# Optimization experiments

Hardware: AMD Instinct MI355X
Metric: run time of the kernel (lower is better)

The kernel has to match this reference:

```python
import jax, jax.numpy as jnp
import numpy as np

D_MODEL = 1024
N_HEADS = 16
D_HEAD = D_MODEL // N_HEADS

def setup_inputs() -> dict:
    key = jax.random.key(0)
    k1, k2, k3 = jax.random.split(key, 3)
    x = jax.random.normal(k1, (4, 2048, D_MODEL), dtype=jnp.float32)
    # Linear weights stored as [in, out] for x @ W
    s = 1.0 / np.sqrt(D_MODEL)
    W_qkv = jax.random.uniform(k2, (D_MODEL, 3 * D_MODEL), jnp.float32, -s, s)
    W_out = jax.random.uniform(k3, (D_MODEL, D_MODEL), jnp.float32, -s, s)
    return {"x": x, "W_qkv": W_qkv, "W_out": W_out}

def reference(x, W_qkv, W_out):
    B, T, C = x.shape
    scale = D_HEAD ** -0.5
    qkv = x @ W_qkv                       # [B,T,3C]
    q, k, v = jnp.split(qkv, 3, axis=-1)
    def heads(t):
        return t.reshape(B, T, N_HEADS, D_HEAD).transpose(0, 2, 1, 3)  # [B,H,T,d]
    q, k, v = heads(q), heads(k), heads(v)
    att = jnp.einsum('bhqd,bhkd->bhqk', q, k) * scale  # [B,H,T,T]
    causal = jnp.tril(jnp.ones((T, T), dtype=bool))
    att = jnp.where(causal, att, -jnp.inf)
    att = jax.nn.softmax(att, axis=-1)
    y = jnp.einsum('bhqk,bhkd->bhqd', att, v)          # [B,H,T,d]
    y = y.transpose(0, 2, 1, 3).reshape(B, T, C)
    return y @ W_out
```

## Files before the change

### kernel.cpp

```cpp
#include <hip/hip_runtime.h>
#include <hip/hip_bf16.h>

typedef unsigned short u16;
typedef __attribute__((ext_vector_type(8))) short short8v;
typedef __attribute__((ext_vector_type(4))) float f32x4;
typedef __attribute__((ext_vector_type(16))) float f32x16;

#define Bb 4
#define Tt 2048
#define Cc 1024
#define Hh 16
#define C3 3072
#define Mm 8192

__device__ __forceinline__ u16 f2bf(float f) {
    union { __hip_bfloat16 h; u16 u; } r;
    r.h = __float2bfloat16(f);
    return r.u;
}
__device__ __forceinline__ unsigned int pk2(float a, float b) {
    union { __hip_bfloat162 h; unsigned int u; } r;
    r.h.x = __float2bfloat16(a);
    r.h.y = __float2bfloat16(b);
    return r.u;
}
__device__ __forceinline__ float exp2g(float x) {
#if __has_builtin(__builtin_amdgcn_exp2f)
    return __builtin_amdgcn_exp2f(x);
#else
    return exp2f(x);
#endif
}
__device__ __forceinline__ void plswap(unsigned int& a, unsigned int& b) {
#if __has_builtin(__builtin_amdgcn_permlane32_swap)
    typedef __attribute__((ext_vector_type(2))) unsigned int uint2v;
    uint2v r = __builtin_amdgcn_permlane32_swap(a, b, false, false);
    a = r.x; b = r.y;
#else
    asm volatile("v_permlane32_swap_b32 %0, %1" : "+v"(a), "+v"(b));
#endif
}
__device__ __forceinline__ void gload16(const void* g, void* l) {
    __builtin_amdgcn_global_load_lds(
        (const __attribute__((address_space(1))) unsigned int*)g,
        (__attribute__((address_space(3))) unsigned int*)l, 16, 0, 0);
}

__global__ __launch_bounds__(256) void cvt_x(const float* __restrict__ in,
                                             u16* __restrict__ out) {
    int i = blockIdx.x * 256 + threadIdx.x;
    float4 v = reinterpret_cast<const float4*>(in)[i];
    ushort4 o;
    o.x = f2bf(v.x); o.y = f2bf(v.y); o.z = f2bf(v.z); o.w = f2bf(v.w);
    reinterpret_cast<ushort4*>(out)[i] = o;
}

__global__ __launch_bounds__(256) void wtrans(const float* __restrict__ in,
                                              u16* __restrict__ out,
                                              int R, int Ccols) {
    __shared__ float t[32][33];
    const int tx = threadIdx.x & 31, ty = threadIdx.x >> 5;
    const int bx = blockIdx.x, by = blockIdx.y;
    const int c = bx * 32 + tx;
#pragma unroll
    for (int j = 0; j < 4; ++j) {
        int r = by * 32 + ty + j * 8;
        t[ty + j * 8][tx] = in[(size_t)r * Ccols + c];
    }
    __syncthreads();
#pragma unroll
    for (int j = 0; j < 4; ++j) {
        int orow = bx * 32 + ty + j * 8;
        int oc   = by * 32 + tx;
        out[(size_t)orow * R + oc] = f2bf(t[tx][ty + j * 8]);
    }
}

template <int MODE>
__global__ __launch_bounds__(256) void gemm_mfma(const u16* __restrict__ A,
                                                 const u16* __restrict__ BT,
                                                 void* __restrict__ C0,
                                                 u16* __restrict__ C1,
                                                 int M, int N, int K) {
    __shared__ u16 As[128 * 32];
    __shared__ u16 Bs[128 * 32];
    const int tid = threadIdx.x;
    const int w = tid >> 6, l = tid & 63;
    const int wr = w >> 1, wc = w & 1;
    const int g = l >> 4, q = l & 15;
    const int bm = blockIdx.x * 128, bn = blockIdx.y * 128;
    const int lrow = l >> 2;
    const int lcol = (l & 3) * 8;

    f32x4 acc[4][4] = {};
    const u16* Ap = A + (size_t)(bm + w * 32 + lrow) * K + lcol;
    const u16* Bp = BT + (size_t)(bn + w * 32 + lrow) * K + lcol;

    for (int k0 = 0; k0 < K; k0 += 32) {
        gload16(Ap + k0, &As[(w * 32) * 32]);
        gload16(Ap + (size_t)16 * K + k0, &As[(w * 32 + 16) * 32]);
        gload16(Bp + k0, &Bs[(w * 32) * 32]);
        gload16(Bp + (size_t)16 * K + k0, &Bs[(w * 32 + 16) * 32]);
        __syncthreads();
        short8v af[4], bf[4];
#pragma unroll
        for (int m = 0; m < 4; ++m)
            af[m] = *reinterpret_cast<const short8v*>(&As[(wr * 64 + m * 16 + q) * 32 + g * 8]);
#pragma unroll
        for (int n = 0; n < 4; ++n)
            bf[n] = *reinterpret_cast<const short8v*>(&Bs[(wc * 64 + n * 16 + q) * 32 + g * 8]);
#pragma unroll
        for (int m = 0; m < 4; ++m)
#pragma unroll
            for (int n = 0; n < 4; ++n)
                acc[m][n] = __builtin_amdgcn_mfma_f32_16x16x32_bf16(af[m], bf[n], acc[m][n], 0, 0, 0);
        __syncthreads();
    }

#pragma unroll
    for (int m = 0; m < 4; ++m)
#pragma unroll
        for (int n = 0; n < 4; ++n) {
            const int col = bn + wc * 64 + n * 16 + q;
#pragma unroll
            for (int r = 0; r < 4; ++r) {
                const int row = bm + wr * 64 + m * 16 + g * 4 + r;
                const float v = acc[m][n][r];
                if (MODE == 1) {
                    reinterpret_cast<float*>(C0)[(size_t)row * N + col] = v;
                } else if (MODE == 0) {
                    reinterpret_cast<u16*>(C0)[(size_t)row * N + col] = f2bf(v);
                } else {
                    if (col < 2048) {
                        reinterpret_cast<u16*>(C0)[(size_t)row * 2048 + col] = f2bf(v);
                    } else {
                        const int bI = row >> 11, tI = row & 2047;
                        C1[((size_t)bI * 1024 + (col - 2048)) * 2048 + tI] = f2bf(v);
                    }
                }
            }
        }
}

__global__ __launch_bounds__(256) void attn_mfma(const u16* __restrict__ qk,
                                                 const u16* __restrict__ vT,
                                                 u16* __restrict__ y) {
    __shared__ u16 SM[18432];
    const int tid = threadIdx.x;
    const int w = tid >> 6, l = tid & 63;
    const int q31 = l & 31, hi = l >> 5;
    const int bid = blockIdx.x;
    const int bh = bid & 63, c0 = bid >> 6;
    const int b = bh >> 4, h = bh & 15;
    const size_t tok0 = (size_t)b * Tt;

    const float C2 = 0.18033688011112042f;
    const float THR = 44.361419555836499f;

    const int srow = tid >> 2;
    const int sseg = (tid & 3) * 16;
    const int soff = srow * 72 + sseg;
    const u16* gK = qk + (tok0 + srow) * 2048 + 1024 + h * 64 + sseg;
    const u16* gV = vT + ((size_t)b * 1024 + h * 64 + srow) * 2048 + sseg;

    for (int phase = 0; phase < 2; ++phase) {
        const int chunk = phase ? (15 - c0) : c0;
        const int nsteps = 2 * (chunk + 1);
        const int q0w = chunk * 128 + w * 32;
        const int qlane = q0w + q31;

        short8v qf0, qf1, qf2, qf3;
        {
            const u16* qp = qk + (tok0 + qlane) * 2048 + h * 64 + hi * 8;
            qf0 = *reinterpret_cast<const short8v*>(qp);
            qf1 = *reinterpret_cast<const short8v*>(qp + 16);
            qf2 = *reinterpret_cast<const short8v*>(qp + 32);
            qf3 = *reinterpret_cast<const short8v*>(qp + 48);
        }

        f32x16 acc0 = {}, acc1 = {};
        float m_run = -1e30f, l_run = 0.f;

        {
            uint4 ka = *reinterpret_cast<const uint4*>(gK);
            uint4 kb = *reinterpret_cast<const uint4*>(gK + 8);
            uint4 va = *reinterpret_cast<const uint4*>(gV);
            uint4 vb = *reinterpret_cast<const uint4*>(gV + 8);
            *reinterpret_cast<uint4*>(&SM[soff]) = ka;
            *reinterpret_cast<uint4*>(&SM[soff + 8]) = kb;
            *reinterpret_cast<uint4*>(&SM[9216 + soff]) = va;
            *reinterpret_cast<uint4*>(&SM[9216 + soff + 8]) = vb;
        }
        __syncthreads();

        for (int t = 0; t < nsteps; ++t) {
            const int cur = t & 1;
            const int k0 = t * 64;
            const bool pre = (t + 1 < nsteps);
            uint4 ka = {}, kb = {}, va = {}, vb = {};
            if (pre) {
                const u16* gKt = gK + (size_t)(t + 1) * 64 * 2048;
                const u16* gVt = gV + (t + 1) * 64;
                ka = *reinterpret_cast<const uint4*>(gKt);
                kb = *reinterpret_cast<const uint4*>(gKt + 8);
                va = *reinterpret_cast<const uint4*>(gVt);
                vb = *reinterpret_cast<const uint4*>(gVt + 8);
            }

            if (k0 <= q0w + 31) {
                const u16* Kb = SM + cur * 4608;
                const u16* Vb = SM + 9216 + cur * 4608;
                f32x16 st0 = {}, st1 = {};
#pragma unroll
                for (int s = 0; s < 4; ++s) {
                    short8v kfa = *reinterpret_cast<const short8v*>(&Kb[q31 * 72 + s * 16 + hi * 8]);
                    short8v kfb = *reinterpret_cast<const short8v*>(&Kb[(q31 + 32) * 72 + s * 16 + hi * 8]);
                    short8v qs = (s == 0) ? qf0 : (s == 1) ? qf1 : (s == 2) ? qf2 : qf3;
                    st0 = __builtin_amdgcn_mfma_f32_32x32x16_bf16(kfa, qs, st0, 0, 0, 0);
                    st1 = __builtin_amdgcn_mfma_f32_32x32x16_bf16(kfb, qs, st1, 0, 0, 0);
                }
                const bool diag = (k0 + 63 > q0w);
                float s0[16], s1[16];
                float mx = -1e30f;
#pragma unroll
                for (int r = 0; r < 16; ++r) {
                    int krel = (r & 3) + 8 * (r >> 2) + 4 * hi;
                    float v0 = st0[r];
                    float v1 = st1[r];
                    if (diag) {
                        if (k0 + krel > qlane) v0 = -1e30f;
                        if (k0 + 32 + krel > qlane) v1 = -1e30f;
                    }
                    s0[r] = v0; s1[r] = v1;
                    mx = fmaxf(mx, fmaxf(v0, v1));
                }
                mx = fmaxf(mx, __shfl_xor(mx, 32));
                if (!__all(mx <= m_run + THR)) {
                    float m_new = fmaxf(m_run, mx);
                    float alpha = exp2g((m_run - m_new) * C2);
                    l_run *= alpha;
                    acc0 *= alpha;
                    acc1 *= alpha;
                    m_run = m_new;
                }
                const float mc = m_run * C2;
                float rs = 0.f;
#pragma unroll
                for (int r = 0; r < 16; ++r) {
                    float p0 = exp2g(fmaf(s0[r], C2, -mc));
                    float p1 = exp2g(fmaf(s1[r], C2, -mc));
                    s0[r] = p0; s1[r] = p1;
                    rs += p0 + p1;
                }
                rs += __shfl_xor(rs, 32);
                l_run += rs;

                short8v pf0, pf1, pf2, pf3;
#define MKFRAG(dst, P, rb)                                                  \
                {                                                           \
                    unsigned int a_ = pk2(P[rb + 0], P[rb + 1]);            \
                    unsigned int b_ = pk2(P[rb + 4], P[rb + 5]);            \
                    unsigned int c_ = pk2(P[rb + 2], P[rb + 3]);            \
                    unsigned int d_ = pk2(P[rb + 6], P[rb + 7]);            \
                    plswap(a_, b_);                                         \
                    plswap(c_, d_);                                         \
                    union { unsigned int u[4]; short8v s; } uf_;            \
                    uf_.u[0] = a_; uf_.u[1] = c_; uf_.u[2] = b_; uf_.u[3] = d_; \
                    dst = uf_.s;                                            \
                }
                MKFRAG(pf0, s0, 0)
                MKFRAG(pf1, s0, 8)
                MKFRAG(pf2, s1, 0)
                MKFRAG(pf3, s1, 8)
#undef MKFRAG
#pragma unroll
                for (int s = 0; s < 4; ++s) {
                    short8v vfa = *reinterpret_cast<const short8v*>(&Vb[q31 * 72 + s * 16 + hi * 8]);
                    short8v vfb = *reinterpret_cast<const short8v*>(&Vb[(q31 + 32) * 72 + s * 16 + hi * 8]);
                    short8v ps = (s == 0) ? pf0 : (s == 1) ? pf1 : (s == 2) ? pf2 : pf3;
                    acc0 = __builtin_amdgcn_mfma_f32_32x32x16_bf16(vfa, ps, acc0, 0, 0, 0);
                    acc1 = __builtin_amdgcn_mfma_f32_32x32x16_bf16(vfb, ps, acc1, 0, 0, 0);
                }
            }

            if (pre) {
                const int nb = cur ^ 1;
                *reinterpret_cast<uint4*>(&SM[nb * 4608 + soff]) = ka;
                *reinterpret_cast<uint4*>(&SM[nb * 4608 + soff + 8]) = kb;
                *reinterpret_cast<uint4*>(&SM[9216 + nb * 4608 + soff]) = va;
                *reinterpret_cast<uint4*>(&SM[9216 + nb * 4608 + soff + 8]) = vb;
            }
            __syncthreads();
        }

        const float inv = 1.f / l_run;
        unsigned int* Od2 = reinterpret_cast<unsigned int*>(SM);
        const int qrow = w * 32 + q31;
#pragma unroll
        for (int r = 0; r < 16; r += 2) {
            int d0 = (r & 3) + 8 * (r >> 2) + 4 * hi;
            Od2[qrow * 36 + (d0 >> 1)] = pk2(acc0[r] * inv, acc0[r + 1] * inv);
            Od2[qrow * 36 + ((32 + d0) >> 1)] = pk2(acc1[r] * inv, acc1[r + 1] * inv);
        }
        __syncthreads();
        {
            const int row = w * 32 + (l >> 1);
            const int dh = (l & 1) * 32;
            const u16* src = SM + row * 72 + dh;
            u16* dst = y + (tok0 + chunk * 128 + row) * Cc + h * 64 + dh;
#pragma unroll
            for (int k2 = 0; k2 < 4; ++k2)
                *reinterpret_cast<uint4*>(dst + k2 * 8) =
                    *reinterpret_cast<const uint4*>(src + k2 * 8);
        }
        __syncthreads();
    }
}

extern "C" void kernel_launch(void* const* d_in, const int* in_sizes, int n_in,
                              void* d_out, int out_size, void* d_ws, size_t ws_size,
                              hipStream_t stream) {
    const float* x    = (const float*)d_in[0];
    const float* Wqkv = (const float*)d_in[1];
    const float* Wout = (const float*)d_in[2];
    float* out = (float*)d_out;

    char* ws = (char*)d_ws;
    u16* qk    = (u16*)(ws);
    u16* vT    = (u16*)(ws + 33554432);
    u16* xbf   = (u16*)(ws + 50331648);
    u16* WqkvT = (u16*)(ws + 67108864);
    u16* WoutT = (u16*)(ws + 73400320);

    cvt_x<<<(Mm * Cc) / (256 * 4), 256, 0, stream>>>(x, xbf);
    wtrans<<<dim3(C3 / 32, Cc / 32), 256, 0, stream>>>(Wqkv, WqkvT, Cc, C3);
    wtrans<<<dim3(Cc / 32, Cc / 32), 256, 0, stream>>>(Wout, WoutT, Cc, Cc);

    gemm_mfma<2><<<dim3(Mm / 128, C3 / 128), 256, 0, stream>>>(xbf, WqkvT, qk, vT, Mm, C3, Cc);

    u16* ybf = xbf;
    attn_mfma<<<512, 256, 0, stream>>>(qk, vT, ybf);

    gemm_mfma<1><<<dim3(Mm / 128, Cc / 128), 256, 0, stream>>>(ybf, WoutT, out, nullptr, Mm, Cc, Cc);
}
```

Baseline: 207.8 us.

## Replace QKV projection GEMM with 256x256-tile, 8-wave double-buffered pipelined kernel

```diff
diff --git a/kernel.cpp b/kernel.cpp
--- a/kernel.cpp
+++ b/kernel.cpp
@@ -76,11 +76,10 @@
     }
 }
 
-template <int MODE>
+template <int OUTF32>
 __global__ __launch_bounds__(256) void gemm_mfma(const u16* __restrict__ A,
                                                  const u16* __restrict__ BT,
                                                  void* __restrict__ C0,
-                                                 u16* __restrict__ C1,
                                                  int M, int N, int K) {
     __shared__ u16 As[128 * 32];
     __shared__ u16 Bs[128 * 32];
@@ -120,23 +119,117 @@
 #pragma unroll
     for (int m = 0; m < 4; ++m)
 #pragma unroll
-        for (int n = 0; n < 4; ++n) {
-            const int col = bn + wc * 64 + n * 16 + q;
+        for (int n = 0; n < 4; ++n)
 #pragma unroll
             for (int r = 0; r < 4; ++r) {
-                const int row = bm + wr * 64 + m * 16 + g * 4 + r;
-                const float v = acc[m][n][r];
-                if (MODE == 1) {
-                    reinterpret_cast<float*>(C0)[(size_t)row * N + col] = v;
-                } else if (MODE == 0) {
-                    reinterpret_cast<u16*>(C0)[(size_t)row * N + col] = f2bf(v);
+                int row = bm + wr * 64 + m * 16 + g * 4 + r;
+                int col = bn + wc * 64 + n * 16 + q;
+                if (OUTF32)
+                    reinterpret_cast<float*>(C0)[(size_t)row * N + col] = acc[m][n][r];
+                else
+                    reinterpret_cast<u16*>(C0)[(size_t)row * N + col] = f2bf(acc[m][n][r]);
+            }
+}
+
+__global__ __launch_bounds__(512, 2) void gemm256_qkv(const u16* __restrict__ A,
+                                                      const u16* __restrict__ BT,
+                                                      u16* __restrict__ qkOut,
+                                                      u16* __restrict__ vTOut,
+                                                      int K) {
+    __shared__ u16 SM[65536];
+    const int tid = threadIdx.x;
+    const int wv = tid >> 6, L = tid & 63;
+    const int wm = wv >> 2, wn = wv & 3;
+    const int q = L & 15, g = L >> 4;
+    const int bm = blockIdx.x * 256, bn = blockIdx.y * 256;
+    const int nK = K >> 6;
+
+    char* smB = (char*)SM;
+    const int srow = wv * 16 + (L >> 3);
+    const int scol = ((L & 7) ^ ((L >> 3) & 7)) * 8;
+    const u16* Asrc = A + (size_t)(bm + srow) * K + scol;
+    const u16* Bsrc = BT + (size_t)(bn + srow) * K + scol;
+
+#define STG2(src, ldsByte)                                                \
+    { gload16((src), smB + (ldsByte) + wv * 2048);                        \
+      gload16((src) + 8 * (size_t)K, smB + (ldsByte) + wv * 2048 + 1024); }
+
+    STG2(Asrc, 0)
+    STG2(Asrc + 128 * (size_t)K, 16384)
+    STG2(Bsrc, 32768)
+    STG2(Bsrc + 128 * (size_t)K, 49152)
+    STG2(Asrc + 64, 65536)
+    STG2(Asrc + 128 * (size_t)K + 64, 65536 + 16384)
+    STG2(Bsrc + 64, 65536 + 32768)
+
+    const int rA = (wm * 128 + q) * 64;
+    const int rB = 16384 + (wn * 64 + q) * 64;
+    const int s0 = (g ^ (q & 7)) * 8;
+    const int s1 = ((4 + g) ^ (q & 7)) * 8;
+
+    f32x4 acc[8][4] = {};
+
+#define MMA(mf, nf)                                                                              \
+    acc[mf][nf] = __builtin_amdgcn_mfma_f32_16x16x32_bf16(Af##mf[0], Bf##nf[0], acc[mf][nf], 0, 0, 0); \
+    acc[mf][nf] = __builtin_amdgcn_mfma_f32_16x16x32_bf16(Af##mf[1], Bf##nf[1], acc[mf][nf], 0, 0, 0);
+#define MBLK(a, b)                                                        \
+    __builtin_amdgcn_s_setprio(1);                                        \
+    MMA(a, 0) MMA(a, 1) MMA(a, 2) MMA(a, 3)                               \
+    MMA(b, 0) MMA(b, 1) MMA(b, 2) MMA(b, 3)                               \
+    __builtin_amdgcn_s_setprio(0);
+
+    for (int t = 0; t < nK; ++t) {
+        const int bufU = (t & 1) * 32768;
+        const int curB = (t & 1) * 65536;
+        const int nxtB = ((t + 1) & 1) * 65536;
+        if (t == nK - 1) { asm volatile("s_waitcnt vmcnt(0)" ::: "memory"); }
+        else             { asm volatile("s_waitcnt vmcnt(6)" ::: "memory"); }
+        __builtin_amdgcn_s_barrier();
+        __builtin_amdgcn_sched_barrier(0);
+
+        short8v Af0[2], Af1[2], Af2[2], Af3[2], Af4[2], Af5[2], Af6[2], Af7[2];
+        short8v Bf0[2], Bf1[2], Bf2[2], Bf3[2];
+#define LDA(mf)                                                                         \
+        Af##mf[0] = *reinterpret_cast<const short8v*>(&SM[bufU + rA + mf * 1024 + s0]); \
+        Af##mf[1] = *reinterpret_cast<const short8v*>(&SM[bufU + rA + mf * 1024 + s1]);
+#define LDB(nf)                                                                         \
+        Bf##nf[0] = *reinterpret_cast<const short8v*>(&SM[bufU + rB + nf * 1024 + s0]); \
+        Bf##nf[1] = *reinterpret_cast<const short8v*>(&SM[bufU + rB + nf * 1024 + s1]);
+        LDA(0) LDA(1) LDA(2) LDA(3) LDA(4) LDA(5) LDA(6) LDA(7)
+        LDB(0) LDB(1) LDB(2) LDB(3)
+#undef LDA
+#undef LDB
+        asm volatile("s_waitcnt lgkmcnt(0)" ::: "memory");
+        __builtin_amdgcn_sched_barrier(0);
+        __builtin_amdgcn_s_barrier();
+
+        if (t + 1 < nK) STG2(Bsrc + 128 * (size_t)K + (t + 1) * 64, nxtB + 49152)
+        MBLK(0, 1)
+        if (t + 2 < nK) STG2(Asrc + (t + 2) * 64, curB)
+        MBLK(2, 3)
+        if (t + 2 < nK) STG2(Asrc + 128 * (size_t)K + (t + 2) * 64, curB + 16384)
+        MBLK(4, 5)
+        if (t + 2 < nK) STG2(Bsrc + (t + 2) * 64, curB + 32768)
+        MBLK(6, 7)
+    }
+#undef MMA
+#undef MBLK
+#undef STG2
+
+#pragma unroll
+    for (int mf = 0; mf < 8; ++mf)
+#pragma unroll
+        for (int nf = 0; nf < 4; ++nf) {
+            const int col = bn + wn * 64 + nf * 16 + q;
+#pragma unroll
+            for (int rr = 0; rr < 4; ++rr) {
+                const int row = bm + wm * 128 + mf * 16 + g * 4 + rr;
+                const u16 v = f2bf(acc[mf][nf][rr]);
+                if (col < 2048) {
+                    qkOut[(size_t)row * 2048 + col] = v;
                 } else {
-                    if (col < 2048) {
-                        reinterpret_cast<u16*>(C0)[(size_t)row * 2048 + col] = f2bf(v);
-                    } else {
-                        const int bI = row >> 11, tI = row & 2047;
-                        C1[((size_t)bI * 1024 + (col - 2048)) * 2048 + tI] = f2bf(v);
-                    }
+                    const int bI = row >> 11, tI = row & 2047;
+                    vTOut[((size_t)bI * 1024 + (col - 2048)) * 2048 + tI] = v;
                 }
             }
         }
@@ -336,10 +429,10 @@
     wtrans<<<dim3(C3 / 32, Cc / 32), 256, 0, stream>>>(Wqkv, WqkvT, Cc, C3);
     wtrans<<<dim3(Cc / 32, Cc / 32), 256, 0, stream>>>(Wout, WoutT, Cc, Cc);
 
-    gemm_mfma<2><<<dim3(Mm / 128, C3 / 128), 256, 0, stream>>>(xbf, WqkvT, qk, vT, Mm, C3, Cc);
+    gemm256_qkv<<<dim3(Mm / 256, C3 / 256), 512, 0, stream>>>(xbf, WqkvT, qk, vT, Cc);
 
     u16* ybf = xbf;
     attn_mfma<<<512, 256, 0, stream>>>(qk, vT, ybf);
 
-    gemm_mfma<1><<<dim3(Mm / 128, Cc / 128), 256, 0, stream>>>(ybf, WoutT, out, nullptr, Mm, Cc, Cc);
-}
+    gemm_mfma<1><<<dim3(Mm / 128, Cc / 128), 256, 0, stream>>>(ybf, WoutT, out, Mm, Cc, Cc);
+}
```

Result: slower. 214.1 us (+3.0%).
